# Kernel tuning notes

Measured on AMD Instinct MI355X. Metric: run time of the kernel, lower is better.

## Reference

```python
import jax, jax.numpy as jnp
import numpy as np

BETA = 15.0   # soft-max temperature used by the soft morphology (logsumexp pooling)
EPS = 1e-5    # BatchNorm eps
BIG = 1e4     # padding value so padded taps vanish in logsumexp


def _soft_morph(x, w, dilation, op):
    """Channel-wise soft morphology. x: (B,C,H,W), w: (C,k,k).
    dilation (erode=False): out = (1/b)*logsumexp_i b*(w_i + x_i)
    erosion: out = -(1/b)*logsumexp_i b*(w_i - x_i)
    """
    C, k, _ = w.shape
    B, _, H, W = x.shape
    pad = dilation * (k - 1) // 2
    pad_val = -BIG if op == 'dil' else BIG
    xp = jnp.pad(x, ((0, 0), (0, 0), (pad, pad), (pad, pad)), constant_values=pad_val)
    taps = []
    for i in range(k):
        for j in range(k):
            patch = xp[:, :, i * dilation:i * dilation + H, j * dilation:j * dilation + W]
            wij = w[:, i, j][None, :, None, None]
            taps.append(wij + patch if op == 'dil' else wij - patch)
    s = jnp.stack(taps, 0)  # (k*k, B, C, H, W)
    out = jax.nn.logsumexp(s * BETA, axis=0) / BETA
    return out if op == 'dil' else -out


def _opening(x, w_ero, w_dil, dilation):
    return _soft_morph(_soft_morph(x, w_ero, dilation, 'ero'), w_dil, dilation, 'dil')


def _bn(x, g, b, m, v):
    scale = (g / jnp.sqrt(v + EPS))[None, :, None, None]
    return (x - m[None, :, None, None]) * scale + b[None, :, None, None]


def setup_inputs() -> dict:
    key = jax.random.key(0)
    ks = jax.random.split(key, 8)
    B, C, H, W, k = 4, 64, 256, 256, 3
    x = jax.random.normal(ks[0], (B, C, H, W), dtype=jnp.float32)
    we = jax.random.normal(ks[1], (4, C, k, k), dtype=jnp.float32) * 0.1   # erosion SEs per branch
    wd = jax.random.normal(ks[2], (4, C, k, k), dtype=jnp.float32) * 0.1   # dilation SEs per branch
    bn_g = jax.random.normal(ks[3], (4, C), dtype=jnp.float32) * 0.1 + 1.0
    bn_b = jax.random.normal(ks[4], (4, C), dtype=jnp.float32) * 0.1
    bn_m = jnp.zeros((4, C), dtype=jnp.float32)
    bn_v = jnp.ones((4, C), dtype=jnp.float32)
    conv_w = jax.random.normal(ks[5], (C, 4 * C), dtype=jnp.float32) * (1.0 / np.sqrt(4 * C))
    bnf_g = jax.random.normal(ks[6], (C,), dtype=jnp.float32) * 0.1 + 1.0
    bnf_b = jax.random.normal(ks[7], (C,), dtype=jnp.float32) * 0.1
    bnf_m = jnp.zeros((C,), dtype=jnp.float32)
    bnf_v = jnp.ones((C,), dtype=jnp.float32)
    return {"x": x, "we": we, "wd": wd, "bn_g": bn_g, "bn_b": bn_b, "bn_m": bn_m,
            "bn_v": bn_v, "conv_w": conv_w, "bnf_g": bnf_g, "bnf_b": bnf_b,
            "bnf_m": bnf_m, "bnf_v": bnf_v}


def reference(x, we, wd, bn_g, bn_b, bn_m, bn_v, conv_w, bnf_g, bnf_b, bnf_m, bnf_v):
    outs = []
    for d in range(4):  # dilations 1..4
        y = _opening(x, we[d], wd[d], d + 1)
        outs.append(jax.nn.relu(_bn(y, bn_g[d], bn_b[d], bn_m[d], bn_v[d])))
    cat = jnp.concatenate(outs, axis=1)             # (B, 4C, H, W)
    z = jnp.einsum('oc,bchw->bohw', conv_w, cat)    # 1x1 conv, no bias
    z = jax.nn.relu(_bn(z, bnf_g, bnf_b, bnf_m, bnf_v))
    return z  # Dropout2d is identity in eval mode
```

## Files before the change

kernel.cpp:

```cpp
#include <hip/hip_runtime.h>
#include <hip/hip_fp16.h>
#include <math.h>


constexpr int C_ = 64, H_ = 256, W_ = 256;
constexpr int HW = H_ * W_;
constexpr float EPSV = 1e-5f;
constexpr float KL2E = 21.64042561333445f;
constexpr float C1   = 0.046209812037329684f;

typedef __attribute__((ext_vector_type(8))) _Float16 half8v;
typedef __attribute__((ext_vector_type(4))) _Float16 half4v;
typedef __attribute__((ext_vector_type(4))) float f32x4;
typedef __attribute__((ext_vector_type(2))) float f32x2;

__device__ _Float16 g_wh[64 * 256];
__device__ float g_scale[64];
__device__ float g_shift[64];
__device__ float g_we9e[4 * 64 * 9];
__device__ float g_wd9e[4 * 64 * 9];
__device__ float g_cs[4 * 64];
__device__ float g_sh[4 * 64];

__global__ __launch_bounds__(256) void prep(
    const float* __restrict__ cw, const float* __restrict__ g,
    const float* __restrict__ bb, const float* __restrict__ bm,
    const float* __restrict__ bv, const float* __restrict__ we,
    const float* __restrict__ wd, const float* __restrict__ bng,
    const float* __restrict__ bnb, const float* __restrict__ bnm,
    const float* __restrict__ bnv)
{
    int i = blockIdx.x * 256 + threadIdx.x;
    g_wh[i] = (_Float16)cw[i];
    if (i < 64) {
        float s = g[i] * rsqrtf(bv[i] + EPSV);
        g_scale[i] = s;
        g_shift[i] = bb[i] - bm[i] * s;
    }
    if (i < 2304) {
        g_we9e[i] = __builtin_amdgcn_exp2f(KL2E * we[i]);
        g_wd9e[i] = __builtin_amdgcn_exp2f(KL2E * wd[i]);
    }
    if (i < 256) {
        float s = bng[i] * rsqrtf(bnv[i] + EPSV);
        g_cs[i] = C1 * s;
        g_sh[i] = bnb[i] - bnm[i] * s;
    }
}

__global__ __launch_bounds__(256) void morph_all(
    const float* __restrict__ x, _Float16* __restrict__ cat)
{
    __shared__ __align__(16) float xs[80 * 92];
    __shared__ __align__(16) float es[72 * 76];
    const int tid = threadIdx.x;
    const int tileW = blockIdx.x & 3, tileH = blockIdx.x >> 2;
    const int c = blockIdx.y, b = blockIdx.z;
    const int h0 = tileH * 64, w0 = tileW * 64;
    const float* xc = x + (b * C_ + c) * HW;

    for (int u = tid; u < 1600; u += 256) {
        int r = u / 20, q4 = (u - r * 20) * 4;
        int gh = h0 - 8 + r, gw = w0 - 8 + q4;
        int ch = min(max(gh, 0), 255), cwi = min(max(gw, 0), 252);
        const float4 v = *(const float4*)&xc[ch * W_ + cwi];
        bool ok = ((unsigned)gh < 256u) && ((unsigned)gw < 253u);
        float4 sv;
        sv.x = ok ? __builtin_amdgcn_exp2f(-KL2E * v.x) : 0.f;
        sv.y = ok ? __builtin_amdgcn_exp2f(-KL2E * v.y) : 0.f;
        sv.z = ok ? __builtin_amdgcn_exp2f(-KL2E * v.z) : 0.f;
        sv.w = ok ? __builtin_amdgcn_exp2f(-KL2E * v.w) : 0.f;
        *(float4*)&xs[r * 92 + q4] = sv;
    }

    #pragma unroll
    for (int d = 0; d < 4; d++) {
        const int D = d + 1;
        const int bc = d * C_ + c;

        float w9[9], wd9[9];
        #pragma unroll
        for (int i = 0; i < 9; i++) {
            w9[i]  = g_we9e[bc * 9 + i];
            wd9[i] = g_wd9e[bc * 9 + i];
        }
        const float cs = g_cs[bc];
        const float shift = g_sh[bc];

        __syncthreads();

        for (int g = tid; g < 360; g += 256) {
            const int col = g / 72;
            const int row = g - col * 72;
            const int qa0 = col * 16;
            float s16[16];
            #pragma unroll
            for (int p = 0; p < 16; p++) s16[p] = 0.f;
            #pragma unroll
            for (int i = 0; i < 3; i++) {
                const f32x4* xr = (const f32x4*)&xs[(row + 4 + (i - 1) * D) * 92 + qa0];
                f32x4 xw[6];
                #pragma unroll
                for (int k = 0; k < 6; k++) xw[k] = xr[k];
                #pragma unroll
                for (int j = 0; j < 3; j++) {
                    const float wv = w9[i * 3 + j];
                    #pragma unroll
                    for (int p = 0; p < 16; p++) {
                        const int wi = (4 - D) + p + j * D;
                        s16[p] = fmaf(wv, xw[wi >> 2][wi & 3], s16[p]);
                    }
                }
            }
            const bool rowok = (unsigned)(h0 + row - 4) < 256u;
            const int gw0 = w0 + qa0 - 4;
            f32x4 ev[4];
            #pragma unroll
            for (int p = 0; p < 16; p++) {
                float gv = __builtin_amdgcn_rcpf(fmaxf(s16[p], 1e-38f));
                bool ok = rowok && ((unsigned)(gw0 + p) < 256u);
                ev[p >> 2][p & 3] = ok ? gv : 0.f;
            }
            f32x4* ep = (f32x4*)&es[row * 76 + qa0];
            ep[0] = ev[0]; ep[1] = ev[1];
            if (qa0 < 64) { ep[2] = ev[2]; ep[3] = ev[3]; }
        }

        __syncthreads();

        {
            const int dr = tid >> 2, dq0 = (tid & 3) * 16;
            float s16[16];
            #pragma unroll
            for (int p = 0; p < 16; p++) s16[p] = 0.f;
            #pragma unroll
            for (int i = 0; i < 3; i++) {
                const f32x4* er = (const f32x4*)&es[(dr + 4 + (i - 1) * D) * 76 + dq0];
                f32x4 ew[6];
                #pragma unroll
                for (int k = 0; k < 6; k++) ew[k] = er[k];
                #pragma unroll
                for (int j = 0; j < 3; j++) {
                    const float wv = wd9[i * 3 + j];
                    #pragma unroll
                    for (int p = 0; p < 16; p++) {
                        const int wi = (4 - D) + p + j * D;
                        s16[p] = fmaf(wv, ew[wi >> 2][wi & 3], s16[p]);
                    }
                }
            }
            half8v hv0, hv1;
            #pragma unroll
            for (int p = 0; p < 16; p++) {
                float y = __builtin_amdgcn_logf(fmaxf(s16[p], 1e-38f)) * cs + shift;
                y = fmaxf(0.f, y);
                if (p < 8) hv0[p] = (_Float16)y; else hv1[p - 8] = (_Float16)y;
            }
            _Float16* cp = &cat[((size_t)((b * 4 + d) * C_ + c)) * HW
                                + (h0 + dr) * W_ + (w0 + dq0)];
            *(half8v*)cp = hv0;
            *(half8v*)(cp + 8) = hv1;
        }
    }
}

__global__ __launch_bounds__(256) void conv_mfma(
    const _Float16* __restrict__ cat, float* __restrict__ out)
{
    __shared__ __align__(16) _Float16 T[2][10240];
    const int tid = threadIdx.x;
    const int lane = tid & 63, wave = tid >> 6;
    const int m = lane & 15, quad = lane >> 4;
    const int b = blockIdx.y;
    const int px0 = blockIdx.x * 256;
    const _Float16* catb = cat + (size_t)b * 256 * HW + px0;

    const int cl2 = lane >> 1, s = lane & 1;
    const int pxw = wave * 64 + s * 8;
    const int wbase = wave * 2560 + (cl2 >> 2) * 80 + (cl2 & 3) * 16 + s * 8;

    const uint t0a = (uint)(uintptr_t)&T[0][0];
    const uint trbase = t0a + wave * 5120 + quad * 320 + m * 8;

    f32x4 acc[4][4];
    #pragma unroll
    for (int ot = 0; ot < 4; ot++)
        #pragma unroll
        for (int pt = 0; pt < 4; pt++)
            acc[ot][pt] = (f32x4){0.f, 0.f, 0.f, 0.f};

    half8v sv[2][4];
    #pragma unroll
    for (int p = 0; p < 4; p++) {
        sv[0][p] = *(const half8v*)&catb[(size_t)cl2 * HW + pxw + p * 16];
        sv[1][p] = *(const half8v*)&catb[(size_t)(32 + cl2) * HW + pxw + p * 16];
    }

    #pragma unroll
    for (int kc = 0; kc < 8; kc++) {
        const int buf = kc & 1;
        const int c0 = kc * 32;
        _Float16* tw = &T[buf][0] + wbase;
        #pragma unroll
        for (int p = 0; p < 4; p++)
            *(half8v*)(tw + p * 640) = sv[buf][p];

        half8v a0 = *(const half8v*)&g_wh[(0  + m) * 256 + c0 + quad * 8];
        half8v a1 = *(const half8v*)&g_wh[(16 + m) * 256 + c0 + quad * 8];
        half8v a2 = *(const half8v*)&g_wh[(32 + m) * 256 + c0 + quad * 8];
        half8v a3 = *(const half8v*)&g_wh[(48 + m) * 256 + c0 + quad * 8];

        if (kc < 6) {
            #pragma unroll
            for (int p = 0; p < 4; p++)
                sv[buf][p] = *(const half8v*)&catb[(size_t)(c0 + 64 + cl2) * HW + pxw + p * 16];
        }

        __builtin_amdgcn_sched_barrier(0);
        asm volatile("s_waitcnt lgkmcnt(0)");
        __builtin_amdgcn_sched_barrier(0);

        const uint tb = trbase + buf * 20480;
        f32x2 trd[4][2];
        #pragma unroll
        for (int pt = 0; pt < 4; pt++) {
            asm volatile("ds_read_b64_tr_b16 %0, %1"
                         : "=v"(trd[pt][0]) : "v"(tb + pt * 1280));
            asm volatile("ds_read_b64_tr_b16 %0, %1"
                         : "=v"(trd[pt][1]) : "v"(tb + pt * 1280 + 160));
        }
        asm volatile("s_waitcnt lgkmcnt(0)");
        __builtin_amdgcn_sched_barrier(0);

        #pragma unroll
        for (int pt = 0; pt < 4; pt++) {
            half4v lo = __builtin_bit_cast(half4v, trd[pt][0]);
            half4v hi = __builtin_bit_cast(half4v, trd[pt][1]);
            half8v bf = __builtin_shufflevector(lo, hi, 0, 1, 2, 3, 4, 5, 6, 7);
            acc[0][pt] = __builtin_amdgcn_mfma_f32_16x16x32_f16(a0, bf, acc[0][pt], 0, 0, 0);
            acc[1][pt] = __builtin_amdgcn_mfma_f32_16x16x32_f16(a1, bf, acc[1][pt], 0, 0, 0);
            acc[2][pt] = __builtin_amdgcn_mfma_f32_16x16x32_f16(a2, bf, acc[2][pt], 0, 0, 0);
            acc[3][pt] = __builtin_amdgcn_mfma_f32_16x16x32_f16(a3, bf, acc[3][pt], 0, 0, 0);
        }
    }

    #pragma unroll
    for (int ot = 0; ot < 4; ot++)
        #pragma unroll
        for (int reg = 0; reg < 4; reg++) {
            const int o = ot * 16 + quad * 4 + reg;
            const float sc = g_scale[o], sh = g_shift[o];
            float* ob = out + ((size_t)(b * 64 + o)) * HW + px0;
            #pragma unroll
            for (int pt = 0; pt < 4; pt++) {
                const int pxl = wave * 64 + pt * 16 + m;
                ob[pxl] = fmaxf(0.f, acc[ot][pt][reg] * sc + sh);
            }
        }
}

extern "C" void kernel_launch(void* const* d_in, const int* in_sizes, int n_in,
                              void* d_out, int out_size, void* d_ws, size_t ws_size,
                              hipStream_t stream)
{
    const float* x   = (const float*)d_in[0];
    const float* we  = (const float*)d_in[1];
    const float* wd  = (const float*)d_in[2];
    const float* bng = (const float*)d_in[3];
    const float* bnb = (const float*)d_in[4];
    const float* bnm = (const float*)d_in[5];
    const float* bnv = (const float*)d_in[6];
    const float* cw  = (const float*)d_in[7];
    const float* fg  = (const float*)d_in[8];
    const float* fb  = (const float*)d_in[9];
    const float* fm  = (const float*)d_in[10];
    const float* fv  = (const float*)d_in[11];
    float* out = (float*)d_out;
    _Float16* cat = (_Float16*)d_ws;

    prep<<<64, 256, 0, stream>>>(cw, fg, fb, fm, fv, we, wd, bng, bnb, bnm, bnv);
    morph_all<<<dim3(16, 64, 4), 256, 0, stream>>>(x, cat);
    conv_mfma<<<dim3(256, 4), 256, 0, stream>>>(cat, out);
}
```

Before: 247.9 us.

## Stage conv input via global_load_lds with triple-buffered pipeline

Replaces the register-staged double buffer in the 1x1-conv MFMA kernel with direct global-to-LDS loads into a three-deep per-wave buffer. Weight fragments are also prefetched two stages ahead, and waits use explicit vmcnt counts. The aim is to skip the VGPR round trip and the LDS store instructions and to keep more loads in flight to hide memory latency. The cost is more LDS per block and fragile hand-tuned waitcnt accounting, because the weight loads also count against vmcnt.

```diff
diff --git a/kernel.cpp b/kernel.cpp
--- a/kernel.cpp
+++ b/kernel.cpp
@@ -13,6 +13,9 @@
 typedef __attribute__((ext_vector_type(4))) _Float16 half4v;
 typedef __attribute__((ext_vector_type(4))) float f32x4;
 typedef __attribute__((ext_vector_type(2))) float f32x2;
+
+typedef const __attribute__((address_space(1))) void gvoid;
+typedef __attribute__((address_space(3))) void svoid;
 
 __device__ _Float16 g_wh[64 * 256];
 __device__ float g_scale[64];
@@ -167,7 +170,7 @@
 __global__ __launch_bounds__(256) void conv_mfma(
     const _Float16* __restrict__ cat, float* __restrict__ out)
 {
-    __shared__ __align__(16) _Float16 T[2][10240];
+    __shared__ __align__(16) _Float16 T[3][4][2048];
     const int tid = threadIdx.x;
     const int lane = tid & 63, wave = tid >> 6;
     const int m = lane & 15, quad = lane >> 4;
@@ -175,12 +178,13 @@
     const int px0 = blockIdx.x * 256;
     const _Float16* catb = cat + (size_t)b * 256 * HW + px0;
 
-    const int cl2 = lane >> 1, s = lane & 1;
-    const int pxw = wave * 64 + s * 8;
-    const int wbase = wave * 2560 + (cl2 >> 2) * 80 + (cl2 & 3) * 16 + s * 8;
-
-    const uint t0a = (uint)(uintptr_t)&T[0][0];
-    const uint trbase = t0a + wave * 5120 + quad * 320 + m * 8;
+    const int c4sel = lane >> 5, p16s = (lane >> 3) & 3;
+    const int chl = (lane >> 1) & 3, halfs = lane & 1;
+    const int ch_in_q = c4sel * 4 + chl;
+    const int px_s = wave * 64 + p16s * 16 + halfs * 8;
+
+    const uint t0a = (uint)(uintptr_t)&T[0][0][0];
+    const uint trlane = (uint)(quad * 1024 + m * 8);
 
     f32x4 acc[4][4];
     #pragma unroll
@@ -189,59 +193,63 @@
         for (int pt = 0; pt < 4; pt++)
             acc[ot][pt] = (f32x4){0.f, 0.f, 0.f, 0.f};
 
-    half8v sv[2][4];
-    #pragma unroll
-    for (int p = 0; p < 4; p++) {
-        sv[0][p] = *(const half8v*)&catb[(size_t)cl2 * HW + pxw + p * 16];
-        sv[1][p] = *(const half8v*)&catb[(size_t)(32 + cl2) * HW + pxw + p * 16];
-    }
-
-    #pragma unroll
-    for (int kc = 0; kc < 8; kc++) {
-        const int buf = kc & 1;
-        const int c0 = kc * 32;
-        _Float16* tw = &T[buf][0] + wbase;
-        #pragma unroll
-        for (int p = 0; p < 4; p++)
-            *(half8v*)(tw + p * 640) = sv[buf][p];
-
-        half8v a0 = *(const half8v*)&g_wh[(0  + m) * 256 + c0 + quad * 8];
-        half8v a1 = *(const half8v*)&g_wh[(16 + m) * 256 + c0 + quad * 8];
-        half8v a2 = *(const half8v*)&g_wh[(32 + m) * 256 + c0 + quad * 8];
-        half8v a3 = *(const half8v*)&g_wh[(48 + m) * 256 + c0 + quad * 8];
-
-        if (kc < 6) {
-            #pragma unroll
-            for (int p = 0; p < 4; p++)
-                sv[buf][p] = *(const half8v*)&catb[(size_t)(c0 + 64 + cl2) * HW + pxw + p * 16];
-        }
-
-        __builtin_amdgcn_sched_barrier(0);
+    half8v a[3][4];
+
+    auto STAGE = [&](int kcs) {
+        #pragma unroll
+        for (int q = 0; q < 4; ++q) {
+            const _Float16* gp = catb + (size_t)(kcs * 32 + q * 8 + ch_in_q) * HW + px_s;
+            __builtin_amdgcn_global_load_lds(
+                (gvoid*)gp, (svoid*)&T[kcs % 3][wave][q * 512], 16, 0, 0);
+        }
+    };
+    auto LOADA = [&](int kcs) {
+        #pragma unroll
+        for (int i = 0; i < 4; ++i)
+            a[kcs % 3][i] = *(const half8v*)&g_wh[(i * 16 + m) * 256 + kcs * 32 + quad * 8];
+    };
+
+    STAGE(0); __builtin_amdgcn_sched_barrier(0);
+    LOADA(0); __builtin_amdgcn_sched_barrier(0);
+    STAGE(1); __builtin_amdgcn_sched_barrier(0);
+    LOADA(1); __builtin_amdgcn_sched_barrier(0);
+    STAGE(2); __builtin_amdgcn_sched_barrier(0);
+
+    #pragma unroll
+    for (int kc = 0; kc < 8; ++kc) {
+        if (kc < 6)       asm volatile("s_waitcnt vmcnt(12)");
+        else if (kc == 6) asm volatile("s_waitcnt vmcnt(8)");
+        else              asm volatile("s_waitcnt vmcnt(0)");
+        __builtin_amdgcn_sched_barrier(0);
+
+        const uint wb = t0a + (uint)(((kc % 3) * 4 + wave) * 4096) + trlane;
+        f32x2 trd[4][2];
+        #pragma unroll
+        for (int pt = 0; pt < 4; ++pt) {
+            asm volatile("ds_read_b64_tr_b16 %0, %1"
+                         : "=v"(trd[pt][0]) : "v"(wb + pt * 128));
+            asm volatile("ds_read_b64_tr_b16 %0, %1"
+                         : "=v"(trd[pt][1]) : "v"(wb + 512 + pt * 128));
+        }
         asm volatile("s_waitcnt lgkmcnt(0)");
         __builtin_amdgcn_sched_barrier(0);
 
-        const uint tb = trbase + buf * 20480;
-        f32x2 trd[4][2];
-        #pragma unroll
-        for (int pt = 0; pt < 4; pt++) {
-            asm volatile("ds_read_b64_tr_b16 %0, %1"
-                         : "=v"(trd[pt][0]) : "v"(tb + pt * 1280));
-            asm volatile("ds_read_b64_tr_b16 %0, %1"
-                         : "=v"(trd[pt][1]) : "v"(tb + pt * 1280 + 160));
-        }
-        asm volatile("s_waitcnt lgkmcnt(0)");
-        __builtin_amdgcn_sched_barrier(0);
-
-        #pragma unroll
-        for (int pt = 0; pt < 4; pt++) {
+        #pragma unroll
+        for (int pt = 0; pt < 4; ++pt) {
             half4v lo = __builtin_bit_cast(half4v, trd[pt][0]);
             half4v hi = __builtin_bit_cast(half4v, trd[pt][1]);
             half8v bf = __builtin_shufflevector(lo, hi, 0, 1, 2, 3, 4, 5, 6, 7);
-            acc[0][pt] = __builtin_amdgcn_mfma_f32_16x16x32_f16(a0, bf, acc[0][pt], 0, 0, 0);
-            acc[1][pt] = __builtin_amdgcn_mfma_f32_16x16x32_f16(a1, bf, acc[1][pt], 0, 0, 0);
-            acc[2][pt] = __builtin_amdgcn_mfma_f32_16x16x32_f16(a2, bf, acc[2][pt], 0, 0, 0);
-            acc[3][pt] = __builtin_amdgcn_mfma_f32_16x16x32_f16(a3, bf, acc[3][pt], 0, 0, 0);
-        }
+            acc[0][pt] = __builtin_amdgcn_mfma_f32_16x16x32_f16(a[kc % 3][0], bf, acc[0][pt], 0, 0, 0);
+            acc[1][pt] = __builtin_amdgcn_mfma_f32_16x16x32_f16(a[kc % 3][1], bf, acc[1][pt], 0, 0, 0);
+            acc[2][pt] = __builtin_amdgcn_mfma_f32_16x16x32_f16(a[kc % 3][2], bf, acc[2][pt], 0, 0, 0);
+            acc[3][pt] = __builtin_amdgcn_mfma_f32_16x16x32_f16(a[kc % 3][3], bf, acc[3][pt], 0, 0, 0);
+        }
+        __builtin_amdgcn_sched_barrier(0);
+
+        if (kc < 6) { LOADA(kc + 2); }
+        __builtin_amdgcn_sched_barrier(0);
+        if (kc < 5) { STAGE(kc + 3); }
+        __builtin_amdgcn_sched_barrier(0);
     }
 
     #pragma unroll
```

Result: no change. 244.9 us (-1.2%).
